# Optimization experiments

Measured on AMD Instinct MI355X. Metric: run time of the kernel, lower is better.

Reference implementation:

```python
import jax, jax.numpy as jnp
import numpy as np

# Fixed by module source: forward hardcodes a 200x200 BEV grid, dim=128,
# MSDeformAttn(n_levels=1, n_heads=4, n_points=8).
B, Z, X, C, H, P = 2, 200, 200, 128, 4, 8
N = Z * X
D = C // H  # head dim = 32


def setup_inputs() -> dict:
    key = jax.random.key(0)
    ks = jax.random.split(key, 12)
    s = 0.02
    return {
        "query": jax.random.normal(ks[0], (B, N, C), jnp.float32),
        # MSDeformAttn.value_proj
        "Wv": jax.random.normal(ks[1], (C, C), jnp.float32) * s,
        "bv": jnp.zeros((C,), jnp.float32),
        # MSDeformAttn.sampling_offsets (C -> H*1*P*2)
        "Woff": jax.random.normal(ks[2], (C, H * P * 2), jnp.float32) * s,
        "boff": jax.random.normal(ks[3], (H * P * 2,), jnp.float32) * 2.0,
        # MSDeformAttn.attention_weights (C -> H*1*P)
        "Wattn": jax.random.normal(ks[4], (C, H * P), jnp.float32) * s,
        "battn": jnp.zeros((H * P,), jnp.float32),
        # MSDeformAttn.output_proj
        "Wout1": jax.random.normal(ks[5], (C, C), jnp.float32) * s,
        "bout1": jnp.zeros((C,), jnp.float32),
        # VanillaSelfAttention.output_proj
        "Wout2": jax.random.normal(ks[6], (C, C), jnp.float32) * s,
        "bout2": jnp.zeros((C,), jnp.float32),
    }


def _forward(query, Wv, bv, Woff, boff, Wattn, battn, Wout1, bout1, Wout2, bout2):
    # Reference points: normalized centers of the 200x200 grid, order (z, x).
    zc = (jnp.arange(Z, dtype=jnp.float32) + 0.5) / Z
    xc = (jnp.arange(X, dtype=jnp.float32) + 0.5) / X
    ref = jnp.stack(jnp.meshgrid(zc, xc, indexing="ij"), axis=-1).reshape(N, 2)

    # value_proj on input_flatten (== query); split heads, lay out as images.
    value = (query @ Wv + bv).reshape(B, Z, X, H, D)
    value_flat = value.transpose(0, 3, 1, 2, 4).reshape(B * H, Z * X, D)  # (BH, ZX, D)

    # Sampling locations: ref + offsets / offset_normalizer ([W, H] = [200, 200]).
    off = (query @ Woff + boff).reshape(B, N, H, P, 2)
    norm = jnp.array([X, Z], jnp.float32)
    loc = ref[None, :, None, None, :] + off / norm  # (B, N, H, P, 2)

    # Attention weights: softmax over n_levels*n_points (= P here).
    attn = jax.nn.softmax((query @ Wattn + battn).reshape(B, N, H, P), axis=-1)

    # grid_sample convention: grid = 2*loc - 1, grid[...,0]=x (width), align_corners=False.
    grid = 2.0 * loc - 1.0
    ix = ((grid[..., 0] + 1.0) * X - 1.0) * 0.5  # pixel x coords
    iy = ((grid[..., 1] + 1.0) * Z - 1.0) * 0.5  # pixel y coords
    ix = ix.transpose(0, 2, 1, 3).reshape(B * H, N * P)
    iy = iy.transpose(0, 2, 1, 3).reshape(B * H, N * P)

    x0f = jnp.floor(ix); y0f = jnp.floor(iy)
    lx = ix - x0f; ly = iy - y0f
    x0 = x0f.astype(jnp.int32); y0 = y0f.astype(jnp.int32)
    x1 = x0 + 1; y1 = y0 + 1

    def corner(xi, yi, w):
        # zero padding: out-of-bounds corners contribute 0
        valid = (xi >= 0) & (xi < X) & (yi >= 0) & (yi < Z)
        idx = jnp.clip(yi, 0, Z - 1) * X + jnp.clip(xi, 0, X - 1)  # (BH, N*P)
        v = jnp.take_along_axis(value_flat, idx[..., None], axis=1)  # (BH, N*P, D)
        return v * (w * valid.astype(w.dtype))[..., None]

    sampled = (
        corner(x0, y0, (1.0 - lx) * (1.0 - ly))
        + corner(x1, y0, lx * (1.0 - ly))
        + corner(x0, y1, (1.0 - lx) * ly)
        + corner(x1, y1, lx * ly)
    ).reshape(B, H, N, P, D)

    # Weighted reduce over points, merge heads.
    out = jnp.einsum("bhnpd,bnhp->bnhd", sampled, attn).reshape(B, N, C)
    out = out @ Wout1 + bout1  # MSDeformAttn.output_proj
    out = out @ Wout2 + bout2  # VanillaSelfAttention.output_proj
    return out + query  # dropout is identity in eval; residual add


def reference(query, Wv, bv, Woff, boff, Wattn, battn, Wout1, bout1, Wout2, bout2):
    return _forward(query, Wv, bv, Woff, boff, Wattn, battn, Wout1, bout1, Wout2, bout2)
```

## Files before the change

### kernel.cpp

```cpp
#include <hip/hip_runtime.h>
#include <hip/hip_bf16.h>
#include <cstddef>

namespace {
constexpr int B  = 2;
constexpr int Z  = 200;
constexpr int X  = 200;
constexpr int C  = 128;
constexpr int H  = 4;
constexpr int P  = 8;
constexpr int N  = Z * X;
constexpr int BN = B * N;
constexpr int SC = 128;
constexpr int NF_P = 14;
constexpr int NF_O = 8;
constexpr int KS   = 4;

typedef __attribute__((ext_vector_type(8))) short short8;
typedef __attribute__((ext_vector_type(4))) float f32x4;
typedef _Float16 h16x2 __attribute__((ext_vector_type(2)));

__device__ inline ushort f2bf(float x) {
    __hip_bfloat16 h = __float2bfloat16(x);
    return *reinterpret_cast<ushort*>(&h);
}
__device__ inline unsigned packbf(float a, float b) {
    return (unsigned)f2bf(a) | ((unsigned)f2bf(b) << 16);
}
__device__ inline ushort f2h(float x) {
    _Float16 h = (_Float16)x;
    return __builtin_bit_cast(ushort, h);
}
__device__ inline float h1f(ushort u) {
    return (float)__builtin_bit_cast(_Float16, u);
}
__device__ inline float2 h2f2(unsigned u) {
    h16x2 h = __builtin_bit_cast(h16x2, u);
    return make_float2((float)h[0], (float)h[1]);
}
__device__ inline unsigned packh(float a, float b) {
    return (unsigned)f2h(a) | ((unsigned)f2h(b) << 16);
}
__device__ inline h16x2 pkrtz(float a, float b) {
    return __builtin_bit_cast(h16x2, __builtin_amdgcn_cvt_pkrtz(a, b));
}
template <int MASK>
__device__ inline float swzx(float x) {
    constexpr int pat = (MASK << 10) | 0x1F;
    return __int_as_float(__builtin_amdgcn_ds_swizzle(__float_as_int(x), pat));
}
template <int MASK>
__device__ inline h16x2 swzh(h16x2 x) {
    constexpr int pat = (MASK << 10) | 0x1F;
    int t = __builtin_amdgcn_ds_swizzle(__builtin_bit_cast(int, x), pat);
    return __builtin_bit_cast(h16x2, t);
}
}

__global__ __launch_bounds__(256) void vsa_k_setup(
    const float* __restrict__ Wv,    const float* __restrict__ bv,
    const float* __restrict__ Woff,  const float* __restrict__ boff,
    const float* __restrict__ Wattn, const float* __restrict__ battn,
    const float* __restrict__ Wout1, const float* __restrict__ bout1,
    const float* __restrict__ Wout2, const float* __restrict__ bout2,
    ushort* __restrict__ wtp, ushort* __restrict__ wtp2,
    float* __restrict__ biasp, float* __restrict__ bias2)
{
    constexpr int NP = KS * NF_P * 64;

    if (blockIdx.x < 65) {
        const int c = threadIdx.x & 127;
        const int k = blockIdx.x * 2 + (threadIdx.x >> 7);
        if (k > 128) return;
        const float* arow = (k < 128) ? (Wout1 + (size_t)k * 128) : bout1;
        float acc = (k < 128) ? 0.f : bout2[c];
        #pragma unroll 4
        for (int j = 0; j < 128; ++j)
            acc = fmaf(arow[j], Wout2[(size_t)j * 128 + c], acc);
        if (k < 128) {
            const int ks = k >> 5;
            const int l  = (((k >> 3) & 3) << 4) | (c & 15);
            const int f  = c >> 4;
            const int t  = (ks * NF_O + f) * 64 + l;
            wtp2[(size_t)t * 8 + (k & 7)] = f2h(acc);
        } else {
            bias2[c] = acc;
        }
        return;
    }

    const int u = (blockIdx.x - 65) * 256 + threadIdx.x;
    if (u < NP) {
        int ks  = u / (NF_P * 64);
        int rem = u - ks * (NF_P * 64);
        int f = rem >> 6, l = rem & 63;
        int n  = f * 16 + (l & 15);
        int kb = ks * 32 + (l >> 4) * 8;
        float v[8];
        #pragma unroll
        for (int e = 0; e < 8; ++e) {
            int k = kb + e;
            if (n < 128)      v[e] = Wv[k * 128 + n];
            else if (n < 192) v[e] = Woff[k * 64 + (n - 128)];
            else              v[e] = Wattn[k * 32 + (n - 192)];
        }
        unsigned* dst = (unsigned*)(wtp + (size_t)u * 8);
        #pragma unroll
        for (int i = 0; i < 4; ++i) dst[i] = packbf(v[2*i], v[2*i+1]);
    } else if (u < NP + 224) {
        int c = u - NP;
        float bb;
        if (c < 128)      bb = bv[c];
        else if (c < 192) bb = boff[c - 128];
        else              bb = battn[c - 192];
        biasp[c] = bb;
    }
}

__global__ __launch_bounds__(512) void vsa_k_proj(
    const float* __restrict__ Q, const ushort* __restrict__ wtp,
    const float* __restrict__ biasp,
    ushort* __restrict__ proj_v16, ushort* __restrict__ proj_s16)
{
    __shared__ ushort lds_wt[KS * NF_P * 64 * 8];

    const int tid  = threadIdx.x;
    const int lane = tid & 63;
    const int wv   = tid >> 6;
    const int row0 = blockIdx.x * 128 + wv * 16;
    const int m  = lane & 15;
    const int kg = lane >> 4;

    {
        const uint4* src = (const uint4*)wtp;
        uint4* dst = (uint4*)lds_wt;
        #pragma unroll
        for (int it = 0; it < 7; ++it)
            dst[it * 512 + tid] = src[it * 512 + tid];
    }
    __syncthreads();

    const float* qp = Q + (size_t)(row0 + m) * 128 + kg * 8;

    f32x4 acc[NF_P];
    #pragma unroll
    for (int f = 0; f < NF_P; ++f) acc[f] = (f32x4){0.f, 0.f, 0.f, 0.f};

    #pragma unroll
    for (int ks = 0; ks < KS; ++ks) {
        float4 a0 = *(const float4*)(qp + ks * 32);
        float4 a1 = *(const float4*)(qp + ks * 32 + 4);
        short8 af;
        af[0] = (short)f2bf(a0.x); af[1] = (short)f2bf(a0.y);
        af[2] = (short)f2bf(a0.z); af[3] = (short)f2bf(a0.w);
        af[4] = (short)f2bf(a1.x); af[5] = (short)f2bf(a1.y);
        af[6] = (short)f2bf(a1.z); af[7] = (short)f2bf(a1.w);
        const short8* wrow = (const short8*)lds_wt + ks * NF_P * 64 + lane;
        #pragma unroll
        for (int f = 0; f < NF_P; ++f)
            acc[f] = __builtin_amdgcn_mfma_f32_16x16x32_bf16(af, wrow[f * 64], acc[f], 0, 0, 0);
    }

    #pragma unroll
    for (int f = 0; f < 8; ++f) {
        const int col = f * 16 + m;
        const float bb = biasp[col];
        #pragma unroll
        for (int r = 0; r < 4; ++r)
            proj_v16[(size_t)(row0 + kg * 4 + r) * 128 + col] = f2h(acc[f][r] + bb);
    }
    #pragma unroll
    for (int f = 8; f < 12; ++f) {
        const int col = f * 16 + m;
        const float bb = biasp[col];
        const int c  = col - 128;
        const int hp = c >> 1, comp = c & 1;
        #pragma unroll
        for (int r = 0; r < 4; ++r)
            proj_s16[(size_t)(row0 + kg * 4 + r) * SC + hp * 4 + comp] = f2h(acc[f][r] + bb);
    }
    #pragma unroll
    for (int f = 12; f < 14; ++f) {
        const float bb = biasp[f * 16 + m];
        const int hp = (f - 12) * 16 + m;
        #pragma unroll
        for (int r = 0; r < 4; ++r) {
            float v = acc[f][r] + bb;
            float mx = v;
            mx = fmaxf(mx, swzx<1>(mx));
            mx = fmaxf(mx, swzx<2>(mx));
            mx = fmaxf(mx, swzx<4>(mx));
            float ex = __expf(v - mx);
            float sm = ex;
            sm += swzx<1>(sm); sm += swzx<2>(sm); sm += swzx<4>(sm);
            const float wp = ex / sm;
            proj_s16[(size_t)(row0 + kg * 4 + r) * SC + hp * 4 + 2] = f2h(wp);
        }
    }
}

__global__ __launch_bounds__(1024) void vsa_k_so(
    const ushort* __restrict__ proj_v16, const ushort* __restrict__ proj_s16,
    const ushort* __restrict__ wtp2, const float* __restrict__ bias2,
    const float* __restrict__ Q, float* __restrict__ out)
{
    __shared__ ushort tmp_lds[16][136];

    const int lane = threadIdx.x & 63;
    const int wv   = threadIdx.x >> 6;
    const int hsub = lane >> 5;
    const int p    = (lane >> 2) & 7;
    const int d8   = lane & 3;

    const int orig = blockIdx.x;
    const int wg   = (orig & 7) * 625 + (orig >> 3);
    const int b    = wg / 2500;
    const int bl0  = (wg - b * 2500) * 16;
    const int i0   = bl0 / 200;
    const int j0   = bl0 - i0 * 200;
    const int bn0  = b * N + bl0;

    const ushort* vb = proj_v16 + (size_t)b * N * 128;
    const int m  = lane & 15;
    const int kg = lane >> 4;
    const int col = (wv & 7) * 16 + m;

    int pix_t[2], h_t[2];
    float fi_t[2], fj_t[2];
    uint2 ow[2];
    #pragma unroll
    for (int t = 0; t < 2; ++t) {
        const int unit = t * 16 + wv;
        const int pix  = unit >> 1;
        pix_t[t] = pix;
        h_t[t]   = (unit & 1) * 2 + hsub;
        const int jr   = j0 + pix;
        const bool wr  = jr >= 200;
        fi_t[t] = (float)(i0 + (wr ? 1 : 0));
        fj_t[t] = (float)(wr ? jr - 200 : jr);
        ow[t] = *(const uint2*)(proj_s16 + (size_t)(bn0 + pix) * SC + (h_t[t] * 8 + p) * 4);
    }

    short8 wfrag[KS];
    float qv[4];
    if (wv < 8) {
        #pragma unroll
        for (int ks = 0; ks < KS; ++ks)
            wfrag[ks] = ((const short8*)wtp2)[ks * NF_O * 64 + wv * 64 + lane];
        #pragma unroll
        for (int r = 0; r < 4; ++r)
            qv[r] = __builtin_nontemporal_load(Q + (size_t)(bn0 + kg * 4 + r) * 128 + col);
    }

    #pragma unroll
    for (int t = 0; t < 2; ++t) {
        const float2 off = h2f2(ow[t].x);
        const float  wp  = h1f((ushort)(ow[t].y & 0xffff));

        const float ixf = fi_t[t] + off.x;
        const float iyf = fj_t[t] + off.y;
        const float x0f = floorf(ixf), y0f = floorf(iyf);
        const float lx = ixf - x0f, ly = iyf - y0f;
        const int x0 = (int)x0f, y0 = (int)y0f;
        const int x1 = x0 + 1,  y1 = y0 + 1;
        const int xc0 = min(max(x0, 0), X - 1), xc1 = min(max(x1, 0), X - 1);
        const int yc0 = min(max(y0, 0), Z - 1), yc1 = min(max(y1, 0), Z - 1);

        const float wx0 = ((unsigned)x0 < (unsigned)X) ? (1.f - lx) : 0.f;
        const float wx1 = ((unsigned)x1 < (unsigned)X) ? lx : 0.f;
        const float wy0 = (((unsigned)y0 < (unsigned)Z) ? (1.f - ly) : 0.f) * wp;
        const float wy1 = (((unsigned)y1 < (unsigned)Z) ? ly : 0.f) * wp;

        const h16x2 w00p = pkrtz(wx0 * wy0, wx0 * wy0);
        const h16x2 w10p = pkrtz(wx1 * wy0, wx1 * wy0);
        const h16x2 w01p = pkrtz(wx0 * wy1, wx0 * wy1);
        const h16x2 w11p = pkrtz(wx1 * wy1, wx1 * wy1);

        const int rb0 = yc0 * X, rb1 = yc1 * X;
        const int hb  = h_t[t] * 32 + d8 * 8;

        const uint4 c00 = *(const uint4*)(vb + (size_t)(rb0 + xc0) * 128 + hb);
        const uint4 c10 = *(const uint4*)(vb + (size_t)(rb0 + xc1) * 128 + hb);
        const uint4 c01 = *(const uint4*)(vb + (size_t)(rb1 + xc0) * 128 + hb);
        const uint4 c11 = *(const uint4*)(vb + (size_t)(rb1 + xc1) * 128 + hb);

        h16x2 a0 = (h16x2)0, a1 = (h16x2)0, a2 = (h16x2)0, a3 = (h16x2)0;
        #define VSA_ACC(c, wpk) { \
            a0 = __builtin_elementwise_fma(__builtin_bit_cast(h16x2, (c).x), wpk, a0); \
            a1 = __builtin_elementwise_fma(__builtin_bit_cast(h16x2, (c).y), wpk, a1); \
            a2 = __builtin_elementwise_fma(__builtin_bit_cast(h16x2, (c).z), wpk, a2); \
            a3 = __builtin_elementwise_fma(__builtin_bit_cast(h16x2, (c).w), wpk, a3); }
        VSA_ACC(c00, w00p)
        VSA_ACC(c10, w10p)
        VSA_ACC(c01, w01p)
        VSA_ACC(c11, w11p)
        #undef VSA_ACC

        a0 += swzh<4>(a0);  a1 += swzh<4>(a1);  a2 += swzh<4>(a2);  a3 += swzh<4>(a3);
        a0 += swzh<8>(a0);  a1 += swzh<8>(a1);  a2 += swzh<8>(a2);  a3 += swzh<8>(a3);
        a0 += swzh<16>(a0); a1 += swzh<16>(a1); a2 += swzh<16>(a2); a3 += swzh<16>(a3);

        if (p == 0) {
            uint4 o;
            o.x = __builtin_bit_cast(unsigned, a0);
            o.y = __builtin_bit_cast(unsigned, a1);
            o.z = __builtin_bit_cast(unsigned, a2);
            o.w = __builtin_bit_cast(unsigned, a3);
            *(uint4*)(&tmp_lds[pix_t[t]][h_t[t] * 32 + d8 * 8]) = o;
        }
    }

    __syncthreads();
    if (wv >= 8) return;

    f32x4 acc = (f32x4){0.f, 0.f, 0.f, 0.f};
    #pragma unroll
    for (int ks = 0; ks < KS; ++ks) {
        short8 af = *(const short8*)(&tmp_lds[m][ks * 32 + kg * 8]);
        acc = __builtin_amdgcn_mfma_f32_16x16x32_f16(af, wfrag[ks], acc, 0, 0, 0);
    }

    const float bb = bias2[col];
    #pragma unroll
    for (int r = 0; r < 4; ++r) {
        const size_t gi = (size_t)(bn0 + kg * 4 + r) * 128 + col;
        __builtin_nontemporal_store(acc[r] + bb + qv[r], out + gi);
    }
}

extern "C" void kernel_launch(void* const* d_in, const int* in_sizes, int n_in,
                              void* d_out, int out_size, void* d_ws, size_t ws_size,
                              hipStream_t stream) {
    const float* Q     = (const float*)d_in[0];
    const float* Wv    = (const float*)d_in[1];
    const float* bv    = (const float*)d_in[2];
    const float* Woff  = (const float*)d_in[3];
    const float* boff  = (const float*)d_in[4];
    const float* Wattn = (const float*)d_in[5];
    const float* battn = (const float*)d_in[6];
    const float* Wout1 = (const float*)d_in[7];
    const float* bout1 = (const float*)d_in[8];
    const float* Wout2 = (const float*)d_in[9];
    const float* bout2 = (const float*)d_in[10];
    float* out = (float*)d_out;

    float*  biasp  = (float*)d_ws;
    float*  bias2  = biasp + 224;
    ushort* proj_s16 = (ushort*)(bias2 + 128);
    ushort* proj_v16 = proj_s16 + (size_t)BN * SC;
    ushort* wtp    = proj_v16 + (size_t)BN * 128;
    ushort* wtp2   = wtp + (size_t)KS * NF_P * 64 * 8;

    constexpr int NP = KS * NF_P * 64;
    constexpr int setup_blocks = 65 + (NP + 224 + 255) / 256;
    vsa_k_setup<<<setup_blocks, 256, 0, stream>>>(
        Wv, bv, Woff, boff, Wattn, battn, Wout1, bout1, Wout2, bout2,
        wtp, wtp2, biasp, bias2);
    vsa_k_proj<<<BN / 128, 512, 0, stream>>>(Q, wtp, biasp, proj_v16, proj_s16);
    vsa_k_so<<<BN / 16, 1024, 0, stream>>>(proj_v16, proj_s16, wtp2, bias2, Q, out);
}
```

Before: 83.51 us.

## Store value projection head-major and gather adjacent x-corners as one 128B read

The projection kernel now writes the value tensor in a per-(batch, head) planar layout (B, H, N, 32) instead of pixel-major with 128 channels. In the sampling kernel each wave handles one head, and adjacent x-corners (s, s+1) are read as one contiguous 64-element span, so each point needs two row loads instead of four scattered loads. The x-weight is picked per half-lane, and the cross-half reduction uses an extra xor-32 shuffle. The aim is to raise cache-line utilisation of the gather, at the cost of a strided store pattern in the projection and extra shuffle work.

```diff
diff --git a/kernel.cpp b/kernel.cpp
--- a/kernel.cpp
+++ b/kernel.cpp
@@ -53,6 +53,10 @@
 __device__ inline h16x2 swzh(h16x2 x) {
     constexpr int pat = (MASK << 10) | 0x1F;
     int t = __builtin_amdgcn_ds_swizzle(__builtin_bit_cast(int, x), pat);
+    return __builtin_bit_cast(h16x2, t);
+}
+__device__ inline h16x2 shflh32(h16x2 x) {
+    int t = __shfl_xor(__builtin_bit_cast(int, x), 32);
     return __builtin_bit_cast(h16x2, t);
 }
 }
@@ -161,13 +165,24 @@
             acc[f] = __builtin_amdgcn_mfma_f32_16x16x32_bf16(af, wrow[f * 64], acc[f], 0, 0, 0);
     }
 
+    size_t vbase[4];
+    #pragma unroll
+    for (int r = 0; r < 4; ++r) {
+        const int row = row0 + kg * 4 + r;
+        const int b_  = (row >= 40000) ? 1 : 0;
+        const int bnl = row - b_ * 40000;
+        vbase[r] = ((size_t)b_ * H * N + bnl) * 32;
+    }
+
     #pragma unroll
     for (int f = 0; f < 8; ++f) {
         const int col = f * 16 + m;
         const float bb = biasp[col];
+        const size_t off_h = (size_t)(f >> 1) * N * 32;
+        const int d = (f & 1) * 16 + m;
         #pragma unroll
         for (int r = 0; r < 4; ++r)
-            proj_v16[(size_t)(row0 + kg * 4 + r) * 128 + col] = f2h(acc[f][r] + bb);
+            proj_v16[vbase[r] + off_h + d] = f2h(acc[f][r] + bb);
     }
     #pragma unroll
     for (int f = 8; f < 12; ++f) {
@@ -208,9 +223,9 @@
 
     const int lane = threadIdx.x & 63;
     const int wv   = threadIdx.x >> 6;
-    const int hsub = lane >> 5;
-    const int p    = (lane >> 2) & 7;
     const int d8   = lane & 3;
+    const int xh   = (lane >> 2) & 1;
+    const int p    = lane >> 3;
 
     const int orig = blockIdx.x;
     const int wg   = (orig & 7) * 625 + (orig >> 3);
@@ -220,25 +235,24 @@
     const int j0   = bl0 - i0 * 200;
     const int bn0  = b * N + bl0;
 
-    const ushort* vb = proj_v16 + (size_t)b * N * 128;
+    const int h = wv & 3;
+    const ushort* vh = proj_v16 + ((size_t)b * H + h) * N * 32;
     const int m  = lane & 15;
     const int kg = lane >> 4;
     const int col = (wv & 7) * 16 + m;
 
-    int pix_t[2], h_t[2];
-    float fi_t[2], fj_t[2];
-    uint2 ow[2];
-    #pragma unroll
-    for (int t = 0; t < 2; ++t) {
-        const int unit = t * 16 + wv;
-        const int pix  = unit >> 1;
+    int pix_t[4];
+    float fi_t[4], fj_t[4];
+    uint2 ow[4];
+    #pragma unroll
+    for (int t = 0; t < 4; ++t) {
+        const int pix = t * 4 + (wv >> 2);
         pix_t[t] = pix;
-        h_t[t]   = (unit & 1) * 2 + hsub;
-        const int jr   = j0 + pix;
-        const bool wr  = jr >= 200;
+        const int jr  = j0 + pix;
+        const bool wr = jr >= 200;
         fi_t[t] = (float)(i0 + (wr ? 1 : 0));
         fj_t[t] = (float)(wr ? jr - 200 : jr);
-        ow[t] = *(const uint2*)(proj_s16 + (size_t)(bn0 + pix) * SC + (h_t[t] * 8 + p) * 4);
+        ow[t] = *(const uint2*)(proj_s16 + (size_t)(bn0 + pix) * SC + (h * 8 + p) * 4);
     }
 
     short8 wfrag[KS];
@@ -253,7 +267,7 @@
     }
 
     #pragma unroll
-    for (int t = 0; t < 2; ++t) {
+    for (int t = 0; t < 4; ++t) {
         const float2 off = h2f2(ow[t].x);
         const float  wp  = h1f((ushort)(ow[t].y & 0xffff));
 
@@ -262,51 +276,48 @@
         const float x0f = floorf(ixf), y0f = floorf(iyf);
         const float lx = ixf - x0f, ly = iyf - y0f;
         const int x0 = (int)x0f, y0 = (int)y0f;
-        const int x1 = x0 + 1,  y1 = y0 + 1;
-        const int xc0 = min(max(x0, 0), X - 1), xc1 = min(max(x1, 0), X - 1);
+        const int y1 = y0 + 1;
+        const int s   = min(max(x0, 0), X - 2);
         const int yc0 = min(max(y0, 0), Z - 1), yc1 = min(max(y1, 0), Z - 1);
 
         const float wx0 = ((unsigned)x0 < (unsigned)X) ? (1.f - lx) : 0.f;
-        const float wx1 = ((unsigned)x1 < (unsigned)X) ? lx : 0.f;
+        const float wx1 = ((unsigned)(x0 + 1) < (unsigned)X) ? lx : 0.f;
+        const int sq = s + xh;
+        const float whalf = (sq == x0) ? wx0 : ((sq == x0 + 1) ? wx1 : 0.f);
+
         const float wy0 = (((unsigned)y0 < (unsigned)Z) ? (1.f - ly) : 0.f) * wp;
         const float wy1 = (((unsigned)y1 < (unsigned)Z) ? ly : 0.f) * wp;
-
-        const h16x2 w00p = pkrtz(wx0 * wy0, wx0 * wy0);
-        const h16x2 w10p = pkrtz(wx1 * wy0, wx1 * wy0);
-        const h16x2 w01p = pkrtz(wx0 * wy1, wx0 * wy1);
-        const h16x2 w11p = pkrtz(wx1 * wy1, wx1 * wy1);
-
-        const int rb0 = yc0 * X, rb1 = yc1 * X;
-        const int hb  = h_t[t] * 32 + d8 * 8;
-
-        const uint4 c00 = *(const uint4*)(vb + (size_t)(rb0 + xc0) * 128 + hb);
-        const uint4 c10 = *(const uint4*)(vb + (size_t)(rb0 + xc1) * 128 + hb);
-        const uint4 c01 = *(const uint4*)(vb + (size_t)(rb1 + xc0) * 128 + hb);
-        const uint4 c11 = *(const uint4*)(vb + (size_t)(rb1 + xc1) * 128 + hb);
-
-        h16x2 a0 = (h16x2)0, a1 = (h16x2)0, a2 = (h16x2)0, a3 = (h16x2)0;
-        #define VSA_ACC(c, wpk) { \
-            a0 = __builtin_elementwise_fma(__builtin_bit_cast(h16x2, (c).x), wpk, a0); \
-            a1 = __builtin_elementwise_fma(__builtin_bit_cast(h16x2, (c).y), wpk, a1); \
-            a2 = __builtin_elementwise_fma(__builtin_bit_cast(h16x2, (c).z), wpk, a2); \
-            a3 = __builtin_elementwise_fma(__builtin_bit_cast(h16x2, (c).w), wpk, a3); }
-        VSA_ACC(c00, w00p)
-        VSA_ACC(c10, w10p)
-        VSA_ACC(c01, w01p)
-        VSA_ACC(c11, w11p)
-        #undef VSA_ACC
+        const float wr0 = whalf * wy0;
+        const float wr1 = whalf * wy1;
+        const h16x2 pk0 = pkrtz(wr0, wr0);
+        const h16x2 pk1 = pkrtz(wr1, wr1);
+
+        const int le = (lane & 7) * 8;
+        const uint4 c0 = *(const uint4*)(vh + (size_t)(yc0 * X + s) * 32 + le);
+        const uint4 c1 = *(const uint4*)(vh + (size_t)(yc1 * X + s) * 32 + le);
+
+        h16x2 a0, a1, a2, a3;
+        a0 = __builtin_bit_cast(h16x2, c0.x) * pk0;
+        a1 = __builtin_bit_cast(h16x2, c0.y) * pk0;
+        a2 = __builtin_bit_cast(h16x2, c0.z) * pk0;
+        a3 = __builtin_bit_cast(h16x2, c0.w) * pk0;
+        a0 = __builtin_elementwise_fma(__builtin_bit_cast(h16x2, c1.x), pk1, a0);
+        a1 = __builtin_elementwise_fma(__builtin_bit_cast(h16x2, c1.y), pk1, a1);
+        a2 = __builtin_elementwise_fma(__builtin_bit_cast(h16x2, c1.z), pk1, a2);
+        a3 = __builtin_elementwise_fma(__builtin_bit_cast(h16x2, c1.w), pk1, a3);
 
         a0 += swzh<4>(a0);  a1 += swzh<4>(a1);  a2 += swzh<4>(a2);  a3 += swzh<4>(a3);
         a0 += swzh<8>(a0);  a1 += swzh<8>(a1);  a2 += swzh<8>(a2);  a3 += swzh<8>(a3);
         a0 += swzh<16>(a0); a1 += swzh<16>(a1); a2 += swzh<16>(a2); a3 += swzh<16>(a3);
-
-        if (p == 0) {
+        a0 += shflh32(a0);  a1 += shflh32(a1);  a2 += shflh32(a2);  a3 += shflh32(a3);
+
+        if (lane < 4) {
             uint4 o;
             o.x = __builtin_bit_cast(unsigned, a0);
             o.y = __builtin_bit_cast(unsigned, a1);
             o.z = __builtin_bit_cast(unsigned, a2);
             o.w = __builtin_bit_cast(unsigned, a3);
-            *(uint4*)(&tmp_lds[pix_t[t]][h_t[t] * 32 + d8 * 8]) = o;
+            *(uint4*)(&tmp_lds[pix_t[t]][h * 32 + d8 * 8]) = o;
         }
     }
 
```

Result: slower. 99.01 us (+18.6%).
